# Kernel tuning notes

Measured on AMD Instinct MI355X. Metric: run time of the kernel, lower is better.

## Reference

```python
import jax, jax.numpy as jnp
import numpy as np

N_NODES = 100000
N_EDGES = 1600000
DIM = 64
N_REL = 8
N_LAYERS = 2


def setup_inputs() -> dict:
    key = jax.random.key(0)
    ks = jax.random.split(key, 6)
    x = jax.random.normal(ks[0], (N_NODES, DIM), dtype=jnp.float32)
    weight = jax.random.normal(ks[1], (N_LAYERS, N_REL, DIM, DIM), dtype=jnp.float32) * (1.0 / np.sqrt(DIM))
    root = jax.random.normal(ks[2], (N_LAYERS, DIM, DIM), dtype=jnp.float32) * (1.0 / np.sqrt(DIM))
    bias = jnp.zeros((N_LAYERS, DIM), dtype=jnp.float32)
    edge_index = jax.random.randint(ks[3], (2, N_EDGES), 0, N_NODES, dtype=jnp.int32)
    edge_type = jax.random.randint(ks[4], (N_EDGES,), 0, N_REL, dtype=jnp.int32)
    return {"x": x, "weight": weight, "root": root, "bias": bias,
            "edge_index": edge_index, "edge_type": edge_type}


def _rgcn_layer(x, W, W_root, b, src, dst, edge_type, num_nodes, num_rel):
    # Per-relation node transform: [R, N, F] (equivalent to per-edge W[etype] @ x_src)
    h = jnp.einsum('nd,rdf->rnf', x, W)
    msg = h[edge_type, src]  # [E, F] relation-indexed gather
    # FastRGCNConv 'mean' aggregation: normalize by per-(dst, relation) edge count
    comb = dst * num_rel + edge_type
    cnt = jax.ops.segment_sum(jnp.ones(src.shape, dtype=x.dtype), comb,
                              num_segments=num_nodes * num_rel)
    norm = 1.0 / jnp.clip(cnt[comb], 1.0)
    agg = jax.ops.segment_sum(msg * norm[:, None], dst, num_segments=num_nodes)
    return agg + x @ W_root + b


def reference(x, weight, root, bias, edge_index, edge_type):
    src, dst = edge_index[0], edge_index[1]
    num_nodes = x.shape[0]
    num_rel = weight.shape[1]
    for l in range(weight.shape[0]):  # stacked RGCN layers, no nonlinearity (as in source)
        x = _rgcn_layer(x, weight[l], root[l], bias[l], src, dst, edge_type,
                        num_nodes, num_rel)
    return x
```

## Files before the change

kernel.cpp:

```cpp
#include <hip/hip_runtime.h>

#define NN    100000
#define NE    1600000
#define DIM   64
#define NREL  8
#define NSEG  (NN * NREL)
#define NTOT  (NSEG + 1)
#define CHUNK 1024
#define NBLK  ((NTOT + CHUNK - 1) / CHUNK)
#define KTOT  (9 * DIM)
#define KAGG  (8 * DIM)
#define APAD  (KTOT + 8)
#define APAD2 (KAGG + 8)
#define ESPMAX (NE + NSEG)
#define SEGB  2048
#define NBUCK ((NSEG + SEGB - 1) / SEGB)
#define BUCKCAP 5120

typedef unsigned short bf16u;
using short8  = __attribute__((ext_vector_type(8))) short;
using bfx4    = __attribute__((ext_vector_type(4))) unsigned short;
using f32x4   = __attribute__((ext_vector_type(4))) float;
using float4v = __attribute__((ext_vector_type(4))) float;

#if defined(__has_builtin)
#if __has_builtin(__builtin_amdgcn_make_buffer_rsrc) && \
    __has_builtin(__builtin_amdgcn_raw_buffer_load_b32) && \
    __has_builtin(__builtin_amdgcn_raw_buffer_store_b32)
#define HAVE_BUF 1
#endif
#endif

#ifdef HAVE_BUF
__device__ __forceinline__ __amdgpu_buffer_rsrc_t mk_rsrc(const void* p, unsigned bytes) {
    return __builtin_amdgcn_make_buffer_rsrc(const_cast<void*>(p), (short)0,
                                             (int)bytes, 0x00020000);
}
#endif

__device__ __forceinline__ bf16u f2bf(float v) {
    unsigned b = __float_as_uint(v);
    return (bf16u)((b + 0x7FFFu + ((b >> 16) & 1u)) >> 16);
}
__device__ __forceinline__ float bf2f(bf16u u) {
    return __uint_as_float((unsigned)u << 16);
}

__device__ __forceinline__ int block_exscan(int v, int* lds) {
    int tid = threadIdx.x;
    lds[tid] = v;
    __syncthreads();
    for (int s = 1; s < (int)blockDim.x; s <<= 1) {
        int t = (tid >= s) ? lds[tid - s] : 0;
        __syncthreads();
        lds[tid] += t;
        __syncthreads();
    }
    return lds[tid] - v;
}

__global__ __launch_bounds__(256) void binit_k(int* __restrict__ bcur) {
    int i = blockIdx.x * 256 + threadIdx.x;
    if (i < NBUCK) bcur[i] = i * BUCKCAP;
}

__global__ __launch_bounds__(256) void part1_k(const int* __restrict__ src,
                                               const int* __restrict__ dst,
                                               const int* __restrict__ et,
                                               int* __restrict__ bcur,
                                               unsigned* __restrict__ tmp) {
    __shared__ int cntl[NBUCK];
    __shared__ int basel[NBUCK];
    for (int i = threadIdx.x; i < NBUCK; i += 256) cntl[i] = 0;
    __syncthreads();
    const int base = blockIdx.x * 2048;
    int cs[8], rs[8]; unsigned pw[8];
#pragma unroll
    for (int j = 0; j < 8; ++j) {
        int i = base + j * 256 + threadIdx.x;
        cs[j] = -1;
        if (i < NE) {
            cs[j] = dst[i] * NREL + et[i];
            pw[j] = ((unsigned)src[i] << 11) | ((unsigned)cs[j] & 2047u);
            rs[j] = atomicAdd(&cntl[cs[j] >> 11], 1);
        }
    }
    __syncthreads();
    for (int i = threadIdx.x; i < NBUCK; i += 256)
        basel[i] = cntl[i] ? atomicAdd(&bcur[i], cntl[i]) : 0;
    __syncthreads();
#pragma unroll
    for (int j = 0; j < 8; ++j)
        if (cs[j] >= 0)
            tmp[basel[cs[j] >> 11] + rs[j]] = pw[j];
}

__global__ __launch_bounds__(256) void ncount_k(const unsigned* __restrict__ tmp,
                                                const int* __restrict__ bcur,
                                                int* __restrict__ cnt) {
    __shared__ int rk[SEGB];
    const int b = blockIdx.x, c0 = b * SEGB;
    const int nsb = min(SEGB, NSEG - c0);
    for (int i = threadIdx.x; i < SEGB; i += 256) rk[i] = 0;
    __syncthreads();
    const int e0 = b * BUCKCAP, e1 = bcur[b];
    for (int e = e0 + threadIdx.x; e < e1; e += 256)
        atomicAdd(&rk[tmp[e] & 2047u], 1);
    __syncthreads();
    for (int i = threadIdx.x; i < nsb; i += 256) cnt[c0 + i] = rk[i];
}

__global__ __launch_bounds__(256) void part2_k(const unsigned* __restrict__ tmp,
                                               const int* __restrict__ bcur,
                                               const int* __restrict__ offp,
                                               int* __restrict__ esp) {
    __shared__ int rk[SEGB];
    const int b = blockIdx.x, c0 = b * SEGB;
    for (int i = threadIdx.x; i < SEGB; i += 256) rk[i] = 0;
    __syncthreads();
    const int e0 = b * BUCKCAP, e1 = bcur[b];
    for (int e = e0 + threadIdx.x; e < e1; e += 256) {
        unsigned w = tmp[e];
        int lc = (int)(w & 2047u);
        int r = atomicAdd(&rk[lc], 1);
        esp[offp[c0 + lc] + r] = (int)(w >> 11);
    }
}

__global__ __launch_bounds__(256) void count_k(const int* __restrict__ dst,
                                               const int* __restrict__ et,
                                               int* __restrict__ cnt, int E) {
    int i = blockIdx.x * 256 + threadIdx.x;
    if (i < E) atomicAdd(&cnt[dst[i] * NREL + et[i]], 1);
}

__global__ __launch_bounds__(256) void scanA_p(const int* __restrict__ cnt,
                                               int* __restrict__ bsum) {
    __shared__ int lds[256];
    int base = blockIdx.x * CHUNK + threadIdx.x * 4;
    int s = 0;
#pragma unroll
    for (int j = 0; j < 4; ++j) {
        int i = base + j;
        if (i < NSEG) { int v = cnt[i]; s += v + (v & 1); }
    }
    int e = block_exscan(s, lds);
    if (threadIdx.x == 255) bsum[blockIdx.x] = e + s;
}

__global__ __launch_bounds__(1024) void scanB(int* __restrict__ bsum) {
    __shared__ int lds[1024];
    int v = (threadIdx.x < NBLK) ? bsum[threadIdx.x] : 0;
    int e = block_exscan(v, lds);
    if (threadIdx.x < NBLK) bsum[threadIdx.x] = e;
}

__global__ __launch_bounds__(256) void scanC_p(const int* __restrict__ cnt,
                                               const int* __restrict__ bsum,
                                               int* __restrict__ offp,
                                               float* __restrict__ inv,
                                               int* __restrict__ esp) {
    __shared__ int lds[256];
    int base = blockIdx.x * CHUNK + threadIdx.x * 4;
    int c4[4], v4[4]; int s = 0;
#pragma unroll
    for (int j = 0; j < 4; ++j) {
        int i = base + j;
        c4[j] = (i < NSEG) ? cnt[i] : 0;
        v4[j] = c4[j] + (c4[j] & 1);
        s += v4[j];
    }
    int e = block_exscan(s, lds) + bsum[blockIdx.x];
#pragma unroll
    for (int j = 0; j < 4; ++j) {
        int i = base + j;
        if (i < NSEG) {
            offp[i] = e;
            inv[i]  = (c4[j] > 0) ? 1.0f / (float)c4[j] : 0.0f;
            if (c4[j] & 1) esp[e + c4[j]] = NN;
            e += v4[j];
        } else if (i == NSEG) { offp[i] = e; }
    }
}

__global__ __launch_bounds__(256) void scanA(const int* __restrict__ cnt,
                                             int* __restrict__ bsum) {
    __shared__ int lds[256];
    int base = blockIdx.x * CHUNK + threadIdx.x * 4;
    int s = 0;
#pragma unroll
    for (int j = 0; j < 4; ++j) { int i = base + j; if (i < NSEG) s += cnt[i]; }
    int e = block_exscan(s, lds);
    if (threadIdx.x == 255) bsum[blockIdx.x] = e + s;
}

__global__ __launch_bounds__(256) void scanC(const int* __restrict__ cnt,
                                             const int* __restrict__ bsum,
                                             int* __restrict__ off,
                                             int* __restrict__ cur) {
    __shared__ int lds[256];
    int base = blockIdx.x * CHUNK + threadIdx.x * 4;
    int v[4]; int s = 0;
#pragma unroll
    for (int j = 0; j < 4; ++j) { int i = base + j; v[j] = (i < NSEG) ? cnt[i] : 0; s += v[j]; }
    int e = block_exscan(s, lds) + bsum[blockIdx.x];
#pragma unroll
    for (int j = 0; j < 4; ++j) {
        int i = base + j;
        if (i < NSEG)       { off[i] = e; cur[i] = e; e += v[j]; }
        else if (i == NSEG) { off[i] = e; }
    }
}

__global__ __launch_bounds__(256) void scatter_k(const int* __restrict__ src,
                                                 const int* __restrict__ dst,
                                                 const int* __restrict__ et,
                                                 int* __restrict__ cur,
                                                 int* __restrict__ es, int E) {
    int i = blockIdx.x * 256 + threadIdx.x;
    if (i < E) {
        int c = dst[i] * NREL + et[i];
        int p = atomicAdd(&cur[c], 1);
        es[p] = src[i];
    }
}

__global__ __launch_bounds__(256) void xcvt_k(const float* __restrict__ x,
                                              bf16u* __restrict__ xb,
                                              bf16u* __restrict__ xb1) {
    int i = blockIdx.x * 256 + threadIdx.x;
    int e4 = i * 4;
    if (e4 < NN * DIM) {
        float4v v = *(const float4v*)(x + e4);
        bfx4 o;
        o.x = f2bf(v.x); o.y = f2bf(v.y); o.z = f2bf(v.z); o.w = f2bf(v.w);
        *(bfx4*)(xb + e4) = o;
    } else if (e4 < (NN + 1) * DIM) {
        bfx4 z = {0, 0, 0, 0};
        *(bfx4*)(xb + e4)  = z;
        *(bfx4*)(xb1 + e4) = z;
    }
}

__global__ __launch_bounds__(256) void btk(const float* __restrict__ W,
                                           const float* __restrict__ R,
                                           bf16u* __restrict__ BtG) {
    int idx = blockIdx.x * 256 + threadIdx.x;
    if (idx >= 2 * DIM * KTOT) return;
    int k = idx % KTOT;
    int n = (idx / KTOT) & (DIM - 1);
    int l = idx / (KTOT * DIM);
    float v;
    if (k < 8 * DIM) v = W[(((size_t)l * NREL + (k >> 6)) * DIM + (k & 63)) * DIM + n];
    else             v = R[((size_t)l * DIM + (k - 8 * DIM)) * DIM + n];
    BtG[idx] = f2bf(v);
}

__global__ __launch_bounds__(256, 8) void agg2_k(
    const bf16u* __restrict__ xb, const int* __restrict__ offp,
    const float* __restrict__ invf, const int* __restrict__ esp,
    bf16u* __restrict__ Ag)
{
    const int lane = threadIdx.x & 63;
    const int wv   = threadIdx.x >> 6;
    const int d0   = (blockIdx.x * 4 + wv) * 8;
    if (d0 >= NN) return;
    const int c0 = d0 * NREL;

#ifdef HAVE_BUF
    const __amdgpu_buffer_rsrc_t xrsrc = mk_rsrc(xb,  (unsigned)((NN + 1) * DIM * 2));
    const __amdgpu_buffer_rsrc_t ersrc = mk_rsrc(esp, (unsigned)(ESPMAX * 4));
    const __amdgpu_buffer_rsrc_t arsrc = mk_rsrc(Ag,  0xFFFFFFFFu);
    const int xoff4 = (lane & 31) * 4;
#define ESLD(pos)  (int)__builtin_amdgcn_raw_buffer_load_b32(ersrc, (pos) * 4, 0, 0)
#define XLD(sv)    __builtin_amdgcn_raw_buffer_load_b32(xrsrc, ((sv) << 7) + xoff4, 0, 0)
#define AGST(pk, seg)                                                          \
    if (lane < 32)                                                             \
        __builtin_amdgcn_raw_buffer_store_b32((pk), arsrc, (lane & 31) * 4,    \
            ((d0 + ((seg) >> 3)) * KAGG + ((seg) & 7) * DIM) * 2, 0);
#else
#define ESLD(pos)  esp[min((pos), ESPMAX - 1)]
#define XLD(sv)    (*(const unsigned*)(xb + (size_t)(sv) * DIM + (lane & 31) * 2))
#define AGST(pk, seg)                                                          \
    if (lane < 32)                                                             \
        *(unsigned*)(Ag + ((size_t)(d0 + ((seg) >> 3)) * KAGG                  \
                           + ((seg) & 7) * DIM + (lane & 31) * 2)) = (pk);
#endif

    int offv = offp[c0 + 1 + lane];
    int invv = ((const int*)invf)[c0 + lane];
    int pBase = __builtin_amdgcn_readfirstlane(offp[c0]);
    int pEnd  = __builtin_amdgcn_readlane(offv, 63);

    int idsbase = pBase;
    int ids     = ESLD(idsbase + lane);
    int ids_nxt = ESLD(idsbase + 64 + lane);

    unsigned q0 = 0, q1 = 0, q2 = 0, q3 = 0, q4 = 0, q5 = 0, q6 = 0, q7 = 0,
             q8 = 0, q9 = 0, qa = 0, qb = 0, qc = 0, qd = 0, qe = 0, qf = 0;
    {
        int pf = pBase;
#define PRIME(Q) if (pf < pEnd) {                                             \
        int idx = pf - idsbase;                                               \
        int sv0 = __builtin_amdgcn_readlane(ids, idx);                        \
        int sv1 = __builtin_amdgcn_readlane(ids, idx + 1);                    \
        int sv  = (lane < 32) ? sv0 : sv1;                                    \
        Q = XLD(sv); }                                                        \
        pf += 2;
        PRIME(q0) PRIME(q1) PRIME(q2) PRIME(q3)
        PRIME(q4) PRIME(q5) PRIME(q6) PRIME(q7)
        PRIME(q8) PRIME(q9) PRIME(qa) PRIME(qb)
        PRIME(qc) PRIME(qd) PRIME(qe) PRIME(qf)
#undef PRIME
    }
    int seg = 0, p = pBase;
    int se      = __builtin_amdgcn_readlane(offv, 0);
    float invn  = __int_as_float(__builtin_amdgcn_readlane(invv, 0));
    float accA = 0.f, accB = 0.f;

#define STEP(Q) {                                                             \
        while (p == se) {             \
            float ta = accA + __shfl_xor(accA, 32);                           \
            float tb = accB + __shfl_xor(accB, 32);                           \
            unsigned pk = (unsigned)f2bf(ta * invn)                           \
                        | ((unsigned)f2bf(tb * invn) << 16);                  \
            AGST(pk, seg)                                                     \
            accA = 0.f; accB = 0.f;                                           \
            if (++seg >= 64) goto agg_done;                                   \
            se   = __builtin_amdgcn_readlane(offv, seg);                      \
            invn = __int_as_float(__builtin_amdgcn_readlane(invv, seg));      \
        }                                                                     \
        accA += __uint_as_float(Q << 16);                                     \
        accB += __uint_as_float(Q & 0xffff0000u);                             \
        int pn = p + 32;                                                      \
        if (pn < pEnd) {                                                      \
            int idx = pn - idsbase;                                           \
            if (idx >= 64) { idsbase = pn;                                    \
                ids = ids_nxt;                                                \
                ids_nxt = ESLD(idsbase + 64 + lane); idx = 0; }               \
            int sv0 = __builtin_amdgcn_readlane(ids, idx);                    \
            int sv1 = __builtin_amdgcn_readlane(ids, idx + 1);                \
            int sv  = (lane < 32) ? sv0 : sv1;                                \
            Q = XLD(sv);                                                      \
        }                                                                     \
        p += 2; }

    for (;;) { STEP(q0) STEP(q1) STEP(q2) STEP(q3)
               STEP(q4) STEP(q5) STEP(q6) STEP(q7)
               STEP(q8) STEP(q9) STEP(qa) STEP(qb)
               STEP(qc) STEP(qd) STEP(qe) STEP(qf) }
agg_done: ;
#undef STEP
#undef ESLD
#undef XLD
#undef AGST
}

template<bool BF16OUT>
__global__ __launch_bounds__(512, 4) void gemm2_k(
    const bf16u* __restrict__ Ag, const bf16u* __restrict__ xb,
    const bf16u* __restrict__ BtG, const float* __restrict__ bias,
    void* __restrict__ outv)
{
    __shared__ bf16u A[64 * APAD2];
    const int tid  = threadIdx.x;
    const int base = blockIdx.x * 64;

    {
        const int srow = tid >> 3, scg = tid & 7;
        const bf16u* gsrc = Ag + (size_t)min(base + srow, NN - 1) * KAGG + scg * 8;
        bf16u* ldst = &A[srow * APAD2 + scg * 8];
#pragma unroll
        for (int j = 0; j < 8; ++j)
            *(short8*)(ldst + j * 64) = *(const short8*)(gsrc + j * 64);
    }
    __syncthreads();

    const int lane = tid & 63, wv = tid >> 6;
    const int l15 = lane & 15, hw = lane >> 4;
    const int tid0 = wv * 2;
    const int tm = tid0 >> 2, tn0 = tid0 & 3;
    const bf16u* Arow = &A[(tm * 16 + l15) * APAD2 + hw * 8];
    const bf16u* xrow = xb + (size_t)min(base + tm * 16 + l15, NN - 1) * DIM + hw * 8;
    const bf16u* B0   = &BtG[(size_t)(tn0 * 16 + l15) * KTOT + hw * 8];
    const bf16u* B1   = B0 + 16 * KTOT;
    f32x4 acc0 = {0.f, 0.f, 0.f, 0.f}, acc1 = {0.f, 0.f, 0.f, 0.f};
#pragma unroll
    for (int ks = 0; ks < KTOT / 32; ++ks) {
        short8 af = (ks < 16) ? *(const short8*)(Arow + ks * 32)
                              : *(const short8*)(xrow + (ks - 16) * 32);
        short8 b0 = *(const short8*)(B0 + ks * 32);
        short8 b1 = *(const short8*)(B1 + ks * 32);
        acc0 = __builtin_amdgcn_mfma_f32_16x16x32_bf16(af, b0, acc0, 0, 0, 0);
        acc1 = __builtin_amdgcn_mfma_f32_16x16x32_bf16(af, b1, acc1, 0, 0, 0);
    }
    int col0 = tn0 * 16 + l15;
    int r0   = tm * 16 + hw * 4;
    float bv0 = bias[col0], bv1 = bias[col0 + 16];
#pragma unroll
    for (int j = 0; j < 4; ++j) {
        int row = base + r0 + j;
        if (row < NN) {
            if constexpr (BF16OUT) {
                bf16u* out = (bf16u*)outv;
                out[(size_t)row * DIM + col0]      = f2bf(acc0[j] + bv0);
                out[(size_t)row * DIM + col0 + 16] = f2bf(acc1[j] + bv1);
            } else {
                float* out = (float*)outv;
                out[(size_t)row * DIM + col0]      = acc0[j] + bv0;
                out[(size_t)row * DIM + col0 + 16] = acc1[j] + bv1;
            }
        }
    }
}

__global__ __launch_bounds__(512, 4) void layer_k(
    const float* __restrict__ xin, const bf16u* __restrict__ BtG,
    const float* __restrict__ bias, const int* __restrict__ off,
    const int* __restrict__ es, float* __restrict__ out)
{
    __shared__ bf16u A[64 * APAD];
    const int lane = threadIdx.x & 63;
    const int wv   = threadIdx.x >> 6;
    const int base = blockIdx.x * 64;
    const int d0   = base + wv * 8;
    const int nds  = min(8, NN - d0);
    bf16u* Aw = &A[wv * 8 * APAD];

    if (nds > 0) {
        const int c0   = d0 * NREL;
        const int nseg = nds * NREL;
        int s1v = off[min(c0 + lane + 1, NSEG)];
        int pBase = off[min(c0, NSEG)];
        pBase = __builtin_amdgcn_readfirstlane(pBase);
        int pEnd  = __builtin_amdgcn_readlane(s1v, nseg - 1);

        float xroot[8];
#pragma unroll
        for (int i = 0; i < 8; ++i)
            xroot[i] = xin[(size_t)min(d0 + i, NN - 1) * DIM + lane];

        int idsbase = pBase;
        int ids = es[min(idsbase + lane, NE - 1)];

        float q0 = 0.f, q1 = 0.f, q2 = 0.f, q3 = 0.f,
              q4 = 0.f, q5 = 0.f, q6 = 0.f, q7 = 0.f;
        {
            int pf = pBase;
#define PRIME(Q) if (pf < pEnd) { int idx = pf - idsbase;                     \
        int sv = __builtin_amdgcn_readlane(ids, idx);                         \
        Q = xin[(size_t)sv * DIM + lane]; } ++pf;
            PRIME(q0) PRIME(q1) PRIME(q2) PRIME(q3)
            PRIME(q4) PRIME(q5) PRIME(q6) PRIME(q7)
#undef PRIME
        }
        int seg = 0, segStart = pBase, p = pBase;
        int se = __builtin_amdgcn_readlane(s1v, 0);
        float acc = 0.f;

#define STEP(Q) {                                                             \
        while (p == se) {                                                     \
            int n = se - segStart;                                            \
            float invn = (n > 0) ? 1.0f / (float)n : 0.f;                     \
            Aw[(seg >> 3) * APAD + (seg & 7) * DIM + lane] = f2bf(acc * invn);\
            acc = 0.f; segStart = p;                                          \
            if (++seg >= nseg) goto agg_done;                                 \
            se = __builtin_amdgcn_readlane(s1v, seg);                         \
        }                                                                     \
        acc += Q;                                                             \
        int pn = p + 8;                                                       \
        if (pn < pEnd) {                                                      \
            int idx = pn - idsbase;                                           \
            if (idx >= 64) { idsbase = pn;                                    \
                ids = es[min(idsbase + lane, NE - 1)]; idx = 0; }             \
            int sv = __builtin_amdgcn_readlane(ids, idx);                     \
            Q = xin[(size_t)sv * DIM + lane];                                 \
        }                                                                     \
        ++p; }

        for (;;) { STEP(q0) STEP(q1) STEP(q2) STEP(q3)
                   STEP(q4) STEP(q5) STEP(q6) STEP(q7) }
agg_done: ;
#undef STEP

#pragma unroll
        for (int i = 0; i < 8; ++i) {
            if (i < nds) Aw[i * APAD + 8 * DIM + lane] = f2bf(xroot[i]);
            else {
#pragma unroll
                for (int r = 0; r < 9; ++r) Aw[i * APAD + r * DIM + lane] = 0;
            }
        }
    } else {
#pragma unroll
        for (int i = 0; i < 8; ++i)
#pragma unroll
            for (int r = 0; r < 9; ++r) Aw[i * APAD + r * DIM + lane] = 0;
    }
    __syncthreads();

    const int l15 = lane & 15, hw = lane >> 4;
    const int tid0 = wv * 2;
    const int tm = tid0 >> 2, tn0 = tid0 & 3;
    const bf16u* Arow = &A[(tm * 16 + l15) * APAD + hw * 8];
    const bf16u* B0   = &BtG[(size_t)(tn0 * 16 + l15) * KTOT + hw * 8];
    const bf16u* B1   = B0 + 16 * KTOT;
    f32x4 acc0 = {0.f, 0.f, 0.f, 0.f}, acc1 = {0.f, 0.f, 0.f, 0.f};
#pragma unroll
    for (int ks = 0; ks < KTOT / 32; ++ks) {
        short8 af = *(const short8*)(Arow + ks * 32);
        short8 b0 = *(const short8*)(B0 + ks * 32);
        short8 b1 = *(const short8*)(B1 + ks * 32);
        acc0 = __builtin_amdgcn_mfma_f32_16x16x32_bf16(af, b0, acc0, 0, 0, 0);
        acc1 = __builtin_amdgcn_mfma_f32_16x16x32_bf16(af, b1, acc1, 0, 0, 0);
    }
    int col0 = tn0 * 16 + l15;
    int r0   = tm * 16 + hw * 4;
    float bv0 = bias[col0], bv1 = bias[col0 + 16];
#pragma unroll
    for (int j = 0; j < 4; ++j) {
        int row = base + r0 + j;
        if (row < NN) {
            out[(size_t)row * DIM + col0]      = acc0[j] + bv0;
            out[(size_t)row * DIM + col0 + 16] = acc1[j] + bv1;
        }
    }
}

__global__ __launch_bounds__(256) void root_k(const float* __restrict__ x,
                                              const float* __restrict__ R,
                                              const float* __restrict__ b,
                                              float* __restrict__ out, int N) {
    int wid  = (blockIdx.x * 256 + threadIdx.x) >> 6;
    int lane = threadIdx.x & 63;
    if (wid >= N) return;
    wid = __builtin_amdgcn_readfirstlane(wid);
    const float* xs = x + (size_t)wid * DIM;
    float acc = b[lane];
#pragma unroll
    for (int k = 0; k < DIM; ++k)
        acc = fmaf(xs[k], R[k * DIM + lane], acc);
    out[(size_t)wid * DIM + lane] = acc;
}

__global__ __launch_bounds__(256) void edge_k(const float* __restrict__ x,
                                              const float* __restrict__ W,
                                              const int* __restrict__ srcv,
                                              const int* __restrict__ dstv,
                                              const int* __restrict__ etv,
                                              const int* __restrict__ cnt,
                                              float* __restrict__ out, int E) {
    int wid  = (blockIdx.x * 256 + threadIdx.x) >> 6;
    int lane = threadIdx.x & 63;
    if (wid >= E) return;
    int s = __builtin_amdgcn_readfirstlane(srcv[wid]);
    int d = __builtin_amdgcn_readfirstlane(dstv[wid]);
    int t = __builtin_amdgcn_readfirstlane(etv[wid]);
    const float* xs = x + (size_t)s * DIM;
    const float* w  = W + (size_t)t * DIM * DIM;
    float acc = 0.f;
#pragma unroll
    for (int k = 0; k < DIM; ++k)
        acc = fmaf(xs[k], w[k * DIM + lane], acc);
    float nrm = 1.0f / fmaxf((float)cnt[d * NREL + t], 1.0f);
    atomicAdd(&out[(size_t)d * DIM + lane], acc * nrm);
}

extern "C" void kernel_launch(void* const* d_in, const int* in_sizes, int n_in,
                              void* d_out, int out_size, void* d_ws, size_t ws_size,
                              hipStream_t stream) {
    const float* x  = (const float*)d_in[0];
    const float* W  = (const float*)d_in[1];
    const float* R  = (const float*)d_in[2];
    const float* B  = (const float*)d_in[3];
    const int*   ei = (const int*)d_in[4];
    const int*   et = (const int*)d_in[5];
    const int* src = ei;
    const int* dst = ei + NE;
    float* out = (float*)d_out;
    char* ws = (char*)d_ws;

    const size_t BIG_WS  = 144160000;
    const size_t FAST_WS = 41604096;

    if (ws_size >= BIG_WS) {
        bf16u* xb0  = (bf16u*)(ws + 0);
        bf16u* xb1  = (bf16u*)(ws + 12800256);
        int*   offp = (int*)  (ws + 25600512);
        float* inv  = (float*)(ws + 28800528);
        int*   esp  = (int*)  (ws + 32000544);
        bf16u* Ag   = (bf16u*)(ws + 41600544);
        int*      cnt = (int*)     (ws + 41600544);
        unsigned* tmp = (unsigned*)(ws + 44800544);
        bf16u* BtG  = (bf16u*)(ws + 144000544);
        int*   bsum = (int*)  (ws + 144148000);
        int*   bcur = (int*)  (ws + 144154368);

        binit_k<<<(NBUCK + 255) / 256, 256, 0, stream>>>(bcur);
        part1_k<<<(NE + 2047) / 2048, 256, 0, stream>>>(src, dst, et, bcur, tmp);
        ncount_k<<<NBUCK, 256, 0, stream>>>(tmp, bcur, cnt);
        scanA_p<<<NBLK, 256, 0, stream>>>(cnt, bsum);
        scanB<<<1, 1024, 0, stream>>>(bsum);
        scanC_p<<<NBLK, 256, 0, stream>>>(cnt, bsum, offp, inv, esp);
        part2_k<<<NBUCK, 256, 0, stream>>>(tmp, bcur, offp, esp);
        btk<<<(2 * DIM * KTOT + 255) / 256, 256, 0, stream>>>(W, R, BtG);
        xcvt_k<<<((NN + 1) * DIM / 4 + 255) / 256, 256, 0, stream>>>(x, xb0, xb1);

        int gblk = (NN + 63) / 64;
        int ablk = NN / 32;
        agg2_k<<<ablk, 256, 0, stream>>>(xb0, offp, inv, esp, Ag);
        gemm2_k<true ><<<gblk, 512, 0, stream>>>(Ag, xb0, BtG, B, (void*)xb1);
        agg2_k<<<ablk, 256, 0, stream>>>(xb1, offp, inv, esp, Ag);
        gemm2_k<false><<<gblk, 512, 0, stream>>>(Ag, xb1, BtG + DIM * KTOT, B + DIM, (void*)out);
    } else if (ws_size >= FAST_WS) {
        float* x1  = (float*)(ws + 0);
        int*   cnt = (int*)  (ws + 25600000);
        int*   off = (int*)  (ws + 28800000);
        int*   cur = (int*)  (ws + 32000016);
        int*   es  = (int*)  (ws + 35200016);
        int*   bsum= (int*)  (ws + 41600016);
        bf16u* BtG = (bf16u*)(ws + 32000016);

        hipMemsetAsync(cnt, 0, sizeof(int) * NSEG, stream);
        count_k<<<(NE + 255) / 256, 256, 0, stream>>>(dst, et, cnt, NE);
        scanA<<<NBLK, 256, 0, stream>>>(cnt, bsum);
        scanB<<<1, 1024, 0, stream>>>(bsum);
        scanC<<<NBLK, 256, 0, stream>>>(cnt, bsum, off, cur);
        scatter_k<<<(NE + 255) / 256, 256, 0, stream>>>(src, dst, et, cur, es, NE);
        btk<<<(2 * DIM * KTOT + 255) / 256, 256, 0, stream>>>(W, R, BtG);

        int nblk = (NN + 63) / 64;
        layer_k<<<nblk, 512, 0, stream>>>(x,  BtG,              B,       off, es, x1);
        layer_k<<<nblk, 512, 0, stream>>>(x1, BtG + DIM * KTOT, B + DIM, off, es, out);
    } else {
        float* x1  = (float*)ws;
        int*   cnt = (int*)(ws + 25600000);
        hipMemsetAsync(cnt, 0, sizeof(int) * NSEG, stream);
        count_k<<<(NE + 255) / 256, 256, 0, stream>>>(dst, et, cnt, NE);
        root_k<<<(NN * 64) / 256 + 1, 256, 0, stream>>>(x, R, B, x1, NN);
        edge_k<<<(NE * 64) / 256, 256, 0, stream>>>(x, W, src, dst, et, cnt, x1, NE);
        root_k<<<(NN * 64) / 256 + 1, 256, 0, stream>>>(x1, R + DIM * DIM, B + DIM, out, NN);
        edge_k<<<(NE * 64) / 256, 256, 0, stream>>>(x1, W + NREL * DIM * DIM, src, dst, et, cnt, out, NE);
    }
}
```

Before: 374.3 us.

## Shrink gemm2 row tile to 32 and use nontemporal Ag traffic

Halves the gemm2 row tile from 64 to 32 nodes per block, so each wave computes a single 16x16 output tile instead of two. This doubles the block count, halves LDS use and raises the launch-bounds occupancy hint to 8. The Ag intermediate is loaded with nontemporal hints, and the store in the aggregation kernel gets a cache-policy bit to keep this streamed buffer from polluting cache. The row bounds checks are dropped because NN is divisible by 32, and each B row is now re-read by twice as many blocks.

```diff
diff --git a/kernel.cpp b/kernel.cpp
--- a/kernel.cpp
+++ b/kernel.cpp
@@ -277,7 +277,7 @@
 #define AGST(pk, seg)                                                          \
     if (lane < 32)                                                             \
         __builtin_amdgcn_raw_buffer_store_b32((pk), arsrc, (lane & 31) * 4,    \
-            ((d0 + ((seg) >> 3)) * KAGG + ((seg) & 7) * DIM) * 2, 0);
+            ((d0 + ((seg) >> 3)) * KAGG + ((seg) & 7) * DIM) * 2, 2 );
 #else
 #define ESLD(pos)  esp[min((pos), ESPMAX - 1)]
 #define XLD(sv)    (*(const unsigned*)(xb + (size_t)(sv) * DIM + (lane & 31) * 2))
@@ -357,59 +357,50 @@
 }
 
 template<bool BF16OUT>
-__global__ __launch_bounds__(512, 4) void gemm2_k(
+__global__ __launch_bounds__(512, 8) void gemm2_k(
     const bf16u* __restrict__ Ag, const bf16u* __restrict__ xb,
     const bf16u* __restrict__ BtG, const float* __restrict__ bias,
     void* __restrict__ outv)
 {
-    __shared__ bf16u A[64 * APAD2];
+    __shared__ bf16u A[32 * APAD2];
     const int tid  = threadIdx.x;
-    const int base = blockIdx.x * 64;
+    const int base = blockIdx.x * 32;
 
     {
-        const int srow = tid >> 3, scg = tid & 7;
-        const bf16u* gsrc = Ag + (size_t)min(base + srow, NN - 1) * KAGG + scg * 8;
+        const int srow = tid >> 4, scg = tid & 15;
+        const bf16u* gsrc = Ag + (size_t)(base + srow) * KAGG + scg * 8;
         bf16u* ldst = &A[srow * APAD2 + scg * 8];
 #pragma unroll
-        for (int j = 0; j < 8; ++j)
-            *(short8*)(ldst + j * 64) = *(const short8*)(gsrc + j * 64);
+        for (int j = 0; j < 4; ++j)
+            *(short8*)(ldst + j * 128) =
+                __builtin_nontemporal_load((const short8*)(gsrc + j * 128));
     }
     __syncthreads();
 
     const int lane = tid & 63, wv = tid >> 6;
     const int l15 = lane & 15, hw = lane >> 4;
-    const int tid0 = wv * 2;
-    const int tm = tid0 >> 2, tn0 = tid0 & 3;
+    const int tm = wv >> 2, tn = wv & 3;
     const bf16u* Arow = &A[(tm * 16 + l15) * APAD2 + hw * 8];
-    const bf16u* xrow = xb + (size_t)min(base + tm * 16 + l15, NN - 1) * DIM + hw * 8;
-    const bf16u* B0   = &BtG[(size_t)(tn0 * 16 + l15) * KTOT + hw * 8];
-    const bf16u* B1   = B0 + 16 * KTOT;
-    f32x4 acc0 = {0.f, 0.f, 0.f, 0.f}, acc1 = {0.f, 0.f, 0.f, 0.f};
+    const bf16u* xrow = xb + (size_t)(base + tm * 16 + l15) * DIM + hw * 8;
+    const bf16u* B0   = &BtG[(size_t)(tn * 16 + l15) * KTOT + hw * 8];
+    f32x4 acc = {0.f, 0.f, 0.f, 0.f};
 #pragma unroll
     for (int ks = 0; ks < KTOT / 32; ++ks) {
         short8 af = (ks < 16) ? *(const short8*)(Arow + ks * 32)
                               : *(const short8*)(xrow + (ks - 16) * 32);
         short8 b0 = *(const short8*)(B0 + ks * 32);
-        short8 b1 = *(const short8*)(B1 + ks * 32);
-        acc0 = __builtin_amdgcn_mfma_f32_16x16x32_bf16(af, b0, acc0, 0, 0, 0);
-        acc1 = __builtin_amdgcn_mfma_f32_16x16x32_bf16(af, b1, acc1, 0, 0, 0);
-    }
-    int col0 = tn0 * 16 + l15;
-    int r0   = tm * 16 + hw * 4;
-    float bv0 = bias[col0], bv1 = bias[col0 + 16];
+        acc = __builtin_amdgcn_mfma_f32_16x16x32_bf16(af, b0, acc, 0, 0, 0);
+    }
+    int col = tn * 16 + l15;
+    int r0  = tm * 16 + hw * 4;
+    float bv = bias[col];
 #pragma unroll
     for (int j = 0; j < 4; ++j) {
         int row = base + r0 + j;
-        if (row < NN) {
-            if constexpr (BF16OUT) {
-                bf16u* out = (bf16u*)outv;
-                out[(size_t)row * DIM + col0]      = f2bf(acc0[j] + bv0);
-                out[(size_t)row * DIM + col0 + 16] = f2bf(acc1[j] + bv1);
-            } else {
-                float* out = (float*)outv;
-                out[(size_t)row * DIM + col0]      = acc0[j] + bv0;
-                out[(size_t)row * DIM + col0 + 16] = acc1[j] + bv1;
-            }
+        if constexpr (BF16OUT) {
+            ((bf16u*)outv)[(size_t)row * DIM + col] = f2bf(acc[j] + bv);
+        } else {
+            ((float*)outv)[(size_t)row * DIM + col] = acc[j] + bv;
         }
     }
 }
@@ -606,7 +597,7 @@
         btk<<<(2 * DIM * KTOT + 255) / 256, 256, 0, stream>>>(W, R, BtG);
         xcvt_k<<<((NN + 1) * DIM / 4 + 255) / 256, 256, 0, stream>>>(x, xb0, xb1);
 
-        int gblk = (NN + 63) / 64;
+        int gblk = NN / 32;
         int ablk = NN / 32;
         agg2_k<<<ablk, 256, 0, stream>>>(xb0, offp, inv, esp, Ag);
         gemm2_k<true ><<<gblk, 512, 0, stream>>>(Ag, xb0, BtG, B, (void*)xb1);
```

Result: slower. 410.5 us (+9.7%).
